# Performance work log

Measured on AMD Instinct MI355X. Metric: run time of the kernel, lower is better.

Reference implementation:

```python
import jax, jax.numpy as jnp
import numpy as np

N = 4096
D = 256
TAU = 0.8
LAM = 0.5
K0, K1 = 64, 128


def setup_inputs() -> dict:
    key = jax.random.key(0)
    ks = jax.random.split(key, 20)
    s = 1.0 / np.sqrt(D)
    pos = (jax.random.uniform(ks[3], (N, N)) < 0.01).astype(jnp.float32)
    pos = pos.at[jnp.arange(N), jnp.arange(N)].set(1.0)  # guarantee a positive per row
    return {
        'z_mp': jax.random.normal(ks[0], (N, D), jnp.float32),
        'z_sc': jax.random.normal(ks[1], (N, D), jnp.float32),
        'feat': jax.random.normal(ks[2], (N, D), jnp.float32),
        'pos': pos,
        'im2c0': jax.random.randint(ks[4], (N,), 0, K0, jnp.int32),
        'im2c1': jax.random.randint(ks[5], (N,), 0, K1, jnp.int32),
        'centroids0': jax.random.normal(ks[6], (K0, D), jnp.float32),
        'centroids1': jax.random.normal(ks[7], (K1, D), jnp.float32),
        'density0': jax.random.uniform(ks[8], (K0,), jnp.float32) + 0.5,
        'density1': jax.random.uniform(ks[9], (K1,), jnp.float32) + 0.5,
        'pW1': jax.random.normal(ks[10], (D, D), jnp.float32) * s * 1.414,
        'pb1': jnp.zeros((D,), jnp.float32),
        'pW2': jax.random.normal(ks[11], (D, D), jnp.float32) * s * 1.414,
        'pb2': jnp.zeros((D,), jnp.float32),
        'mW1': jax.random.normal(ks[12], (D, D), jnp.float32) * s,
        'mb1': jnp.zeros((D,), jnp.float32),
        'mW2': jax.random.normal(ks[13], (D, D), jnp.float32) * s,
        'mb2': jnp.zeros((D,), jnp.float32),
    }


def _mlp(x, W1, b1, W2, b2):
    # nn.Linear -> ELU -> nn.Linear (torch Linear: x @ W.T + b)
    return jax.nn.elu(x @ W1.T + b1) @ W2.T + b2


def _sim(z1, z2, tau):
    n1 = jnp.linalg.norm(z1, axis=-1, keepdims=True)
    n2 = jnp.linalg.norm(z2, axis=-1, keepdims=True)
    return jnp.exp((z1 @ z2.T) / (n1 @ n2.T) / tau)


def _nce(sim_matrix, pos):
    m = sim_matrix / (sim_matrix.sum(axis=1, keepdims=True) + 1e-8)
    return -jnp.log((m * pos).sum(axis=-1)).mean()


def _pocl(z_anchor, z, im2cs, centroids, densities):
    n = z_anchor.shape[0]
    # weight[a,b] = #levels where a,b share a cluster (original: coo @ coo.T summed)
    sames = [(c[:, None] == c[None, :]).astype(z.dtype) for c in im2cs]
    weight = sames[0] + sames[1]
    node_prototypes = jnp.zeros_like(z)
    loss = jnp.float32(0.0)
    for same, im2c, protos, dens in zip(sames, im2cs, centroids, densities):
        # original aliases weight_clus = weight, so masking accumulates in-place
        weight = weight * same
        c = (weight @ z) / weight.sum(axis=1)[:, None]
        node_prototypes = node_prototypes + 0.1 * c
        phi = dens[im2c]
        pos_p = jnp.exp((z_anchor * node_prototypes).sum(axis=1) / phi)
        neg_p = jnp.exp((z_anchor @ protos.T) / dens).mean(axis=1) * n
        loss = loss + (-jnp.log(pos_p / neg_p)).mean()
    return loss / len(im2cs)


def reference(z_mp, z_sc, feat, pos, im2c0, im2c1, centroids0, centroids1,
              density0, density1, pW1, pb1, pW2, pb2, mW1, mb1, mW2, mb2):
    z_proj_mp = _mlp(z_mp, pW1, pb1, pW2, pb2)
    z_proj_sc = _mlp(z_sc, pW1, pb1, pW2, pb2)
    m_mp2sc = _sim(z_proj_mp, z_proj_sc, TAU)
    lori_mp = _nce(m_mp2sc, pos)
    lori_sc = _nce(m_mp2sc.T, pos)
    proto_loss = _pocl(z_sc, z_mp, [im2c0, im2c1],
                       [centroids0, centroids1], [density0, density1])
    mp_intra = _mlp(z_mp, mW1, mb1, mW2, mb2)
    loss_intramp = _nce(_sim(mp_intra, mp_intra, 0.05), pos)
    proj_mp_feat = _mlp(z_mp, pW1, pb1, pW2, pb2)
    proj_feat = _mlp(feat, pW1, pb1, pW2, pb2)
    lori_mpfeat = _nce(_sim(proj_mp_feat, proj_feat, TAU), pos)
    lori_featmp = _nce(_sim(proj_feat, proj_mp_feat, TAU), pos)
    return (LAM * lori_mp + (1 - LAM) * lori_sc + 0.3 * loss_intramp
            + proto_loss + 0.01 * lori_mpfeat + 0.01 * lori_featmp)
```

## Files before the change

### kernel.cpp

```cpp
#include <hip/hip_runtime.h>
#include <math.h>


#define NROWS 4096
#define DIM   256
#define ND    ((size_t)NROWS * DIM)

typedef unsigned short u16;
typedef unsigned int   u32;
typedef unsigned long long u64;
typedef __attribute__((ext_vector_type(8))) short bf16x8;
typedef __attribute__((ext_vector_type(4))) float f32x4;

__device__ __forceinline__ u16 f2bf(float f) {
    u32 u = __float_as_uint(f);
    return (u16)((u + 0x7fffu + ((u >> 16) & 1u)) >> 16);
}
__device__ __forceinline__ float bf2f(u16 h) {
    return __uint_as_float(((u32)h) << 16);
}

__device__ __forceinline__ void gload16(const u16* g, u16* l) {
    __builtin_amdgcn_global_load_lds(
        (const __attribute__((address_space(1))) u32*)g,
        (__attribute__((address_space(3))) u32*)l, 16, 0, 0);
}

template<int ROWS>
__device__ __forceinline__ void stage_panel(const u16* P, int kk, u16* S, int tid) {
#pragma unroll
    for (int p = 0; p < ROWS / 64; ++p) {
        const int ch = p * 256 + tid, row = ch >> 2, seg = ch & 3;
        gload16(P + (size_t)row * DIM + kk + seg * 8, &S[ch * 8]);
    }
}

__device__ __forceinline__ void wait_lgkm0() {
    asm volatile("s_waitcnt lgkmcnt(0)" ::: "memory");
    __builtin_amdgcn_sched_barrier(0);
}
template<int N> __device__ __forceinline__ void wait_vm() {
    if constexpr (N == 0)      asm volatile("s_waitcnt vmcnt(0)" ::: "memory");
    else if constexpr (N == 3) asm volatile("s_waitcnt vmcnt(3)" ::: "memory");
    else if constexpr (N == 4) asm volatile("s_waitcnt vmcnt(4)" ::: "memory");
    else if constexpr (N == 6) asm volatile("s_waitcnt vmcnt(6)" ::: "memory");
}

struct Ptr3 { const float* s0; const float* s1; const float* s2; };
__global__ __launch_bounds__(256) void cvt_in(Ptr3 p, u16* __restrict__ dst)
{
    const int z = blockIdx.y;
    const float* s = z == 0 ? p.s0 : (z == 1 ? p.s1 : p.s2);
    u16* d = dst + (size_t)z * ND;
    const int i = blockIdx.x * 256 + threadIdx.x;
    const float4 v = ((const float4*)s)[i];
    ushort4 o;
    o.x = f2bf(v.x); o.y = f2bf(v.y); o.z = f2bf(v.z); o.w = f2bf(v.w);
    ((ushort4*)d)[i] = o;
}
struct Ptr4 { const float* s0; const float* s1; const float* s2; const float* s3; };
__global__ __launch_bounds__(256) void cvt_w(Ptr4 p, u16* __restrict__ dst)
{
    const int z = blockIdx.y;
    const float* s = z == 0 ? p.s0 : (z == 1 ? p.s1 : (z == 2 ? p.s2 : p.s3));
    u16* d = dst + (size_t)z * 65536;
    const int i = blockIdx.x * 256 + threadIdx.x;
    const float4 v = ((const float4*)s)[i];
    ushort4 o;
    o.x = f2bf(v.x); o.y = f2bf(v.y); o.z = f2bf(v.z); o.w = f2bf(v.w);
    ((ushort4*)d)[i] = o;
}
__global__ __launch_bounds__(256) void cvt_cent(const float* __restrict__ c0,
                                                const float* __restrict__ c1,
                                                u16* __restrict__ CB)
{
    const int i = blockIdx.x * 256 + threadIdx.x;
    const float4 v = (i < 4096) ? ((const float4*)c0)[i]
                                : ((const float4*)c1)[i - 4096];
    ushort4 o;
    o.x = f2bf(v.x); o.y = f2bf(v.y); o.z = f2bf(v.z); o.w = f2bf(v.w);
    ((ushort4*)CB)[i] = o;
}

__global__ __launch_bounds__(256) void posbits(const float* __restrict__ pos,
                                               u64* __restrict__ bits)
{
    const int i = blockIdx.x;
    const int w = threadIdx.x >> 6, l = threadIdx.x & 63;
#pragma unroll
    for (int c = 0; c < 16; ++c) {
        const int j = c * 256 + w * 64 + l;
        const float v = pos[(size_t)i * NROWS + j];
        const u64 m = __ballot(v != 0.f);
        if (l == 0) bits[(size_t)i * 64 + c * 4 + w] = m;
    }
}

template<int ACT, int REMAP>
__global__ __launch_bounds__(256, 4) void mlp_mfma(const u16* __restrict__ IN,
                                                   const u16* __restrict__ Wp,
                                                   const u16* __restrict__ Wm,
                                                   const float* __restrict__ bp,
                                                   const float* __restrict__ bm,
                                                   u16* __restrict__ OUT)
{
    __shared__ __align__(16) u16 As[3][64 * 32];
    __shared__ __align__(16) u16 Bs[3][128 * 32];
    const int tid = threadIdx.x;
    const int bx = blockIdx.x, by = blockIdx.y;
    const bool intra = by >= 192;
    const int arow = (REMAP && intra) ? (by - 192) * 64 : by * 64;
    const u16* A = IN + (size_t)arow * DIM;
    const u16* B = (intra ? Wm : Wp) + (size_t)(bx * 128) * DIM;
    const float* bias = intra ? bm : bp;
    const int l = tid & 63, w = tid >> 6, wr = w >> 1, wc = w & 1;
    const int lr = l & 15, lk = l >> 4;

    f32x4 acc[2][4] = {};
    stage_panel<64>(A, 0, As[0], tid);
    stage_panel<128>(B, 0, Bs[0], tid);
    stage_panel<64>(A, 32, As[1], tid);
    stage_panel<128>(B, 32, Bs[1], tid);
    wait_vm<3>();
    __builtin_amdgcn_s_barrier();
#pragma unroll
    for (int t = 0; t < 8; ++t) {
        bf16x8 a[2], b[4];
#pragma unroll
        for (int mi = 0; mi < 2; ++mi)
            a[mi] = *(const bf16x8*)&As[t % 3][(wr * 32 + mi * 16 + lr) * 32 + lk * 8];
#pragma unroll
        for (int ni = 0; ni < 4; ++ni)
            b[ni] = *(const bf16x8*)&Bs[t % 3][(wc * 64 + ni * 16 + lr) * 32 + lk * 8];
        if (t < 6) {
            stage_panel<64>(A, (t + 2) * 32, As[(t + 2) % 3], tid);
            stage_panel<128>(B, (t + 2) * 32, Bs[(t + 2) % 3], tid);
        }
        wait_lgkm0();
#pragma unroll
        for (int mi = 0; mi < 2; ++mi)
#pragma unroll
            for (int ni = 0; ni < 4; ++ni)
                acc[mi][ni] = __builtin_amdgcn_mfma_f32_16x16x32_bf16(a[mi], b[ni], acc[mi][ni], 0, 0, 0);
        if (t < 6)      { wait_vm<3>(); __builtin_amdgcn_s_barrier(); }
        else if (t < 7) { wait_vm<0>(); __builtin_amdgcn_s_barrier(); }
    }

    const int j0 = bx * 128;
    float bv[4];
#pragma unroll
    for (int ni = 0; ni < 4; ++ni) bv[ni] = bias[j0 + wc * 64 + ni * 16 + lr];
#pragma unroll
    for (int mi = 0; mi < 2; ++mi)
#pragma unroll
        for (int r = 0; r < 4; ++r) {
            const int row = by * 64 + wr * 32 + mi * 16 + lk * 4 + r;
#pragma unroll
            for (int ni = 0; ni < 4; ++ni) {
                float v = acc[mi][ni][r] + bv[ni];
                if (ACT) v = v > 0.f ? v : expm1f(v);
                OUT[(size_t)row * DIM + j0 + wc * 64 + ni * 16 + lr] = f2bf(v);
            }
        }
}

__global__ __launch_bounds__(256) void rownorm_bf(u16* __restrict__ X)
{
    const int w = threadIdx.x >> 6, l = threadIdx.x & 63;
    const int row = blockIdx.x * 4 + w;
    ushort4* p = (ushort4*)(X + (size_t)row * DIM) + l;
    ushort4 u = *p;
    const float a = bf2f(u.x), b = bf2f(u.y), c = bf2f(u.z), d = bf2f(u.w);
    float ss = a * a + b * b + c * c + d * d;
#pragma unroll
    for (int m = 1; m < 64; m <<= 1) ss += __shfl_xor(ss, m);
    const float inv = rsqrtf(ss);
    u.x = f2bf(a * inv); u.y = f2bf(b * inv); u.z = f2bf(c * inv); u.w = f2bf(d * inv);
    *p = u;
}

__global__ __launch_bounds__(256, 3) void simstat3c(const u16* __restrict__ PROJ,
                                                    const u64* __restrict__ bits,
                                                    float* __restrict__ ST)
{
    const int bid = blockIdx.x;
    int z, by, bx;
    if (bid < 1024) {
        z = 0;
        const int x = bid & 7, j = bid >> 3;
        by = (x >> 1) * 8 + (j >> 4);
        bx = (x & 1) * 16 + (j & 15);
    } else if (bid < 1552) {
        z = 1;
        const int u = bid - 1024;
        const int t = (u & 7) * 66 + (u >> 3);
        int r = (int)((65.0f - sqrtf(4225.0f - 8.0f * (float)t)) * 0.5f);
        int off = 32 * r - (r * (r - 1)) / 2;
        if (t < off)                   { --r; off -= 33 - r; }
        else if (t >= off + (32 - r))  { off += 32 - r; ++r; }
        by = r; bx = r + (t - off);
    } else {
        z = 2;
        const int v = bid - 1552;
        const int x = v & 7, j = v >> 3;
        by = (x >> 1) * 8 + (j >> 4);
        bx = (x & 1) * 16 + (j & 15);
    }

    __shared__ __align__(16) u16 As[3][128 * 32];
    __shared__ __align__(16) u16 Bs[3][128 * 32];
    const int tid = threadIdx.x;
    int ao, bo;
    float* rsr; float* rsc;
    switch (z) {
        case 0:  ao = 0; bo = 1; rsr = ST + 0;     rsc = ST + 8192;  break;
        case 1:  ao = 3; bo = 3; rsr = ST + 16384; rsc = ST + 16384; break;
        default: ao = 0; bo = 2; rsr = ST + 24576; rsc = ST + 32768; break;
    }
    const float invtau = (z == 1) ? 20.f : 1.25f;
    const bool docol = (z != 1) || (bx > by);
    const int i0 = by * 128, j0 = bx * 128;
    const u16* A = PROJ + (size_t)ao * ND + (size_t)i0 * DIM;
    const u16* B = PROJ + (size_t)bo * ND + (size_t)j0 * DIM;
    const int l = tid & 63, w = tid >> 6, wr = w >> 1, wc = w & 1;
    const int lr = l & 15, lk = l >> 4;

    f32x4 acc[4][4] = {};
    stage_panel<128>(A, 0, As[0], tid);
    stage_panel<128>(B, 0, Bs[0], tid);
    stage_panel<128>(A, 32, As[1], tid);
    stage_panel<128>(B, 32, Bs[1], tid);
    wait_vm<4>();
    __builtin_amdgcn_s_barrier();
#pragma unroll
    for (int t = 0; t < 8; ++t) {
        bf16x8 a[4], b[4];
#pragma unroll
        for (int mi = 0; mi < 4; ++mi)
            a[mi] = *(const bf16x8*)&As[t % 3][(wr * 64 + mi * 16 + lr) * 32 + lk * 8];
#pragma unroll
        for (int ni = 0; ni < 4; ++ni)
            b[ni] = *(const bf16x8*)&Bs[t % 3][(wc * 64 + ni * 16 + lr) * 32 + lk * 8];
        if (t < 6) {
            stage_panel<128>(A, (t + 2) * 32, As[(t + 2) % 3], tid);
            stage_panel<128>(B, (t + 2) * 32, Bs[(t + 2) % 3], tid);
        }
        wait_lgkm0();
#pragma unroll
        for (int mi = 0; mi < 4; ++mi)
#pragma unroll
            for (int ni = 0; ni < 4; ++ni)
                acc[mi][ni] = __builtin_amdgcn_mfma_f32_16x16x32_bf16(a[mi], b[ni], acc[mi][ni], 0, 0, 0);
        if (t < 6)      { wait_vm<4>(); __builtin_amdgcn_s_barrier(); }
        else if (t < 7) { wait_vm<0>(); __builtin_amdgcn_s_barrier(); }
    }

#pragma unroll
    for (int mi = 0; mi < 4; ++mi)
#pragma unroll
        for (int ni = 0; ni < 4; ++ni)
#pragma unroll
            for (int r = 0; r < 4; ++r)
                acc[mi][ni][r] = __expf(acc[mi][ni][r] * invtau);

#pragma unroll
    for (int mi = 0; mi < 4; ++mi)
#pragma unroll
        for (int r = 0; r < 4; ++r) {
            const int i = i0 + wr * 64 + mi * 16 + lk * 4 + r;
            const u64 pw = bits[(size_t)i * 64 + bx * 2 + wc];
            float rsum = 0.f, psum = 0.f;
#pragma unroll
            for (int ni = 0; ni < 4; ++ni) {
                const float ev = acc[mi][ni][r];
                rsum += ev;
                psum += ((pw >> (ni * 16 + lr)) & 1ull) ? ev : 0.f;
            }
#pragma unroll
            for (int m = 1; m < 16; m <<= 1) {
                rsum += __shfl_xor(rsum, m);
                psum += __shfl_xor(psum, m);
            }
            if (lr == 0) {
                atomicAdd(&rsr[i], rsum);
                atomicAdd(&rsr[4096 + i], psum);
            }
        }

    if (docol) {
#pragma unroll
        for (int ni = 0; ni < 4; ++ni) {
            const int j = j0 + wc * 64 + ni * 16 + lr;
            const u64 pw = bits[(size_t)j * 64 + by * 2 + wr];
            float csum = 0.f, qsum = 0.f;
#pragma unroll
            for (int mi = 0; mi < 4; ++mi)
#pragma unroll
                for (int r = 0; r < 4; ++r) {
                    const float ev = acc[mi][ni][r];
                    csum += ev;
                    qsum += ((pw >> (mi * 16 + lk * 4 + r)) & 1ull) ? ev : 0.f;
                }
            csum += __shfl_xor(csum, 16); csum += __shfl_xor(csum, 32);
            qsum += __shfl_xor(qsum, 16); qsum += __shfl_xor(qsum, 32);
            if (lk == 0) {
                atomicAdd(&rsc[j], csum);
                atomicAdd(&rsc[4096 + j], qsum);
            }
        }
    }
}

__global__ __launch_bounds__(256, 4) void gcent_mfma(const u16* __restrict__ Zb,
                                                     const u16* __restrict__ CB,
                                                     float* __restrict__ G)
{
    __shared__ __align__(16) u16 As[3][128 * 32];
    __shared__ __align__(16) u16 Bs[3][64 * 32];
    const int tid = threadIdx.x;
    const int bx = blockIdx.x, by = blockIdx.y;
    const int i0 = by * 128, j0 = bx * 64;
    const u16* A = Zb + (size_t)i0 * DIM;
    const u16* B = CB + (size_t)j0 * DIM;
    const int l = tid & 63, w = tid >> 6, wr = w >> 1, wc = w & 1;
    const int lr = l & 15, lk = l >> 4;

    f32x4 acc[4][2] = {};
    stage_panel<128>(A, 0, As[0], tid);
    stage_panel<64>(B, 0, Bs[0], tid);
    stage_panel<128>(A, 32, As[1], tid);
    stage_panel<64>(B, 32, Bs[1], tid);
    wait_vm<3>();
    __builtin_amdgcn_s_barrier();
#pragma unroll
    for (int t = 0; t < 8; ++t) {
        bf16x8 a[4], b[2];
#pragma unroll
        for (int mi = 0; mi < 4; ++mi)
            a[mi] = *(const bf16x8*)&As[t % 3][(wr * 64 + mi * 16 + lr) * 32 + lk * 8];
#pragma unroll
        for (int ni = 0; ni < 2; ++ni)
            b[ni] = *(const bf16x8*)&Bs[t % 3][(wc * 32 + ni * 16 + lr) * 32 + lk * 8];
        if (t < 6) {
            stage_panel<128>(A, (t + 2) * 32, As[(t + 2) % 3], tid);
            stage_panel<64>(B, (t + 2) * 32, Bs[(t + 2) % 3], tid);
        }
        wait_lgkm0();
#pragma unroll
        for (int mi = 0; mi < 4; ++mi)
#pragma unroll
            for (int ni = 0; ni < 2; ++ni)
                acc[mi][ni] = __builtin_amdgcn_mfma_f32_16x16x32_bf16(a[mi], b[ni], acc[mi][ni], 0, 0, 0);
        if (t < 6)      { wait_vm<3>(); __builtin_amdgcn_s_barrier(); }
        else if (t < 7) { wait_vm<0>(); __builtin_amdgcn_s_barrier(); }
    }

#pragma unroll
    for (int mi = 0; mi < 4; ++mi)
#pragma unroll
        for (int r = 0; r < 4; ++r) {
            const int row = i0 + wr * 64 + mi * 16 + lk * 4 + r;
#pragma unroll
            for (int ni = 0; ni < 2; ++ni)
                G[(size_t)row * 192 + j0 + wc * 32 + ni * 16 + lr] = acc[mi][ni][r];
        }
}

__global__ __launch_bounds__(256) void scatter_pairs(const float* __restrict__ z,
                                                     const int* __restrict__ i0a,
                                                     const int* __restrict__ i1a,
                                                     float* __restrict__ S01,
                                                     float* __restrict__ cnt01)
{
    const int b = blockIdx.x, d = threadIdx.x;
    const int p = i0a[b] * 128 + i1a[b];
    atomicAdd(&S01[(size_t)p * DIM + d], z[(size_t)b * DIM + d]);
    if (d == 0) atomicAdd(&cnt01[p], 1.f);
}

__global__ __launch_bounds__(256) void reduce_pairs(const float* __restrict__ S01,
                                                    const float* __restrict__ cnt01,
                                                    float* __restrict__ S0,
                                                    float* __restrict__ cnt0)
{
    const int k0 = blockIdx.x, d = threadIdx.x;
    float s = 0.f;
    for (int k1 = 0; k1 < 128; ++k1)
        s += S01[(size_t)(k0 * 128 + k1) * DIM + d];
    S0[(size_t)k0 * DIM + d] = s;
    __shared__ float c[128];
    if (d < 128) c[d] = cnt01[k0 * 128 + d];
    __syncthreads();
    if (d == 0) {
        float t = 0.f;
        for (int i = 0; i < 128; ++i) t += c[i];
        cnt0[k0] = t;
    }
}

__global__ __launch_bounds__(256) void pocl_row(const float* __restrict__ z_sc,
                                                const int* __restrict__ i0a,
                                                const int* __restrict__ i1a,
                                                const float* __restrict__ S0,
                                                const float* __restrict__ S01,
                                                const float* __restrict__ cnt0,
                                                const float* __restrict__ cnt01,
                                                const float* __restrict__ G,
                                                const float* __restrict__ d0,
                                                const float* __restrict__ d1,
                                                float* __restrict__ L1,
                                                float* __restrict__ L2)
{
    const int w = threadIdx.x >> 6, l = threadIdx.x & 63;
    const int a = blockIdx.x * 4 + w;
    const int k0 = i0a[a], k1 = i1a[a];
    const int p = k0 * 128 + k1;
    const float n0 = cnt0[k0], n01 = cnt01[p];
    const float inv1 = 1.f / (n0 + n01), inv2 = 1.f / n01;
    const float4 s0  = *(const float4*)&S0[(size_t)k0 * DIM + l * 4];
    const float4 s01 = *(const float4*)&S01[(size_t)p * DIM + l * 4];
    const float4 zd  = *(const float4*)&z_sc[(size_t)a * DIM + l * 4];

    float dot1 = 0.f, dot2 = 0.f;
    {
        const float c1x = (s0.x + s01.x) * inv1, c2x = s01.x * inv2;
        const float c1y = (s0.y + s01.y) * inv1, c2y = s01.y * inv2;
        const float c1z = (s0.z + s01.z) * inv1, c2z = s01.z * inv2;
        const float c1w = (s0.w + s01.w) * inv1, c2w = s01.w * inv2;
        dot1 = zd.x * c1x + zd.y * c1y + zd.z * c1z + zd.w * c1w;
        dot2 = zd.x * (c1x + c2x) + zd.y * (c1y + c2y) + zd.z * (c1z + c2z) + zd.w * (c1w + c2w);
    }
    dot1 *= 0.1f; dot2 *= 0.1f;
#pragma unroll
    for (int m = 1; m < 64; m <<= 1) {
        dot1 += __shfl_xor(dot1, m);
        dot2 += __shfl_xor(dot2, m);
    }

    const float x0 = G[(size_t)a * 192 + l] / d0[l];
    float M0 = x0;
#pragma unroll
    for (int m = 1; m < 64; m <<= 1) M0 = fmaxf(M0, __shfl_xor(M0, m));
    float e0 = __expf(x0 - M0);
#pragma unroll
    for (int m = 1; m < 64; m <<= 1) e0 += __shfl_xor(e0, m);

    const float x1a = G[(size_t)a * 192 + 64 + l] / d1[l];
    const float x1b = G[(size_t)a * 192 + 128 + l] / d1[64 + l];
    float M1 = fmaxf(x1a, x1b);
#pragma unroll
    for (int m = 1; m < 64; m <<= 1) M1 = fmaxf(M1, __shfl_xor(M1, m));
    float e1 = __expf(x1a - M1) + __expf(x1b - M1);
#pragma unroll
    for (int m = 1; m < 64; m <<= 1) e1 += __shfl_xor(e1, m);

    if (l == 0) {
        const float lneg1 = M0 + logf(e0) - logf(64.f)  + logf(4096.f);
        const float lneg2 = M1 + logf(e1) - logf(128.f) + logf(4096.f);
        L1[a] = lneg1 - dot1 / d0[k0];
        L2[a] = lneg2 - dot2 / d1[k1];
    }
}

__global__ __launch_bounds__(256) void final_reduce(const float* __restrict__ st,
                                                    const float* __restrict__ L1,
                                                    const float* __restrict__ L2,
                                                    float* __restrict__ out)
{
    const int t = threadIdx.x;
    const float* rs0 = st + 0;      const float* pr0 = st + 4096;
    const float* rs1 = st + 8192;   const float* pr1 = st + 12288;
    const float* rs2 = st + 16384;  const float* pr2 = st + 20480;
    const float* rs3 = st + 24576;  const float* pr3 = st + 28672;
    const float* rs4 = st + 32768;  const float* pr4 = st + 36864;

    float acc = 0.f;
    for (int i = t; i < NROWS; i += 256) {
        const float lmp = logf(rs0[i] + 1e-8f) - logf(pr0[i]);
        const float lsc = logf(rs1[i] + 1e-8f) - logf(pr1[i]);
        const float lin = logf(rs2[i] + 1e-8f) - logf(pr2[i]);
        const float lmf = logf(rs3[i] + 1e-8f) - logf(pr3[i]);
        const float lfm = logf(rs4[i] + 1e-8f) - logf(pr4[i]);
        acc += 0.5f * (lmp + lsc) + 0.3f * lin
             + 0.01f * (lmf + lfm) + 0.5f * (L1[i] + L2[i]);
    }
    __shared__ float red[256];
    red[t] = acc; __syncthreads();
    for (int s = 128; s > 0; s >>= 1) {
        if (t < s) red[t] += red[t + s];
        __syncthreads();
    }
    if (t == 0) out[0] = red[0] * (1.f / 4096.f);
}

extern "C" void kernel_launch(void* const* d_in, const int* in_sizes, int n_in,
                              void* d_out, int out_size, void* d_ws, size_t ws_size,
                              hipStream_t stream)
{
    const float* z_mp = (const float*)d_in[0];
    const float* z_sc = (const float*)d_in[1];
    const float* feat = (const float*)d_in[2];
    const float* pos  = (const float*)d_in[3];
    const int*   im0  = (const int*)d_in[4];
    const int*   im1  = (const int*)d_in[5];
    const float* c0   = (const float*)d_in[6];
    const float* c1   = (const float*)d_in[7];
    const float* d0   = (const float*)d_in[8];
    const float* d1   = (const float*)d_in[9];
    const float* pW1  = (const float*)d_in[10];
    const float* pb1  = (const float*)d_in[11];
    const float* pW2  = (const float*)d_in[12];
    const float* pb2  = (const float*)d_in[13];
    const float* mW1  = (const float*)d_in[14];
    const float* mb1  = (const float*)d_in[15];
    const float* mW2  = (const float*)d_in[16];
    const float* mb2  = (const float*)d_in[17];
    float* out = (float*)d_out;
    float* ws  = (float*)d_ws;
    (void)in_sizes; (void)n_in; (void)out_size; (void)ws_size;

    float* ST   = ws;
    float* S0f  = ST + 40960;
    float* CN0  = S0f + 16384;
    float* CN01 = CN0 + 64;
    float* S01f = CN01 + 8192;
    float* ZEND = S01f + (size_t)8192 * DIM;
    float* G    = ZEND;
    float* L1   = G + (size_t)NROWS * 192;
    float* L2   = L1 + NROWS;
    u64*  bits  = (u64*)(L2 + NROWS);
    u16*  INb   = (u16*)(bits + (size_t)NROWS * 64);
    u16*  Hb    = INb + 3 * ND;
    u16*  PROJ  = Hb + 4 * ND;
    u16*  Wb    = PROJ + 4 * ND;
    u16*  CB    = Wb + 4 * 65536;

    hipMemsetAsync(ws, 0, (size_t)(ZEND - ws) * sizeof(float), stream);

    const dim3 blk(256);

    Ptr3 pin{z_mp, z_sc, feat};
    cvt_in<<<dim3(1024, 3), blk, 0, stream>>>(pin, INb);
    Ptr4 pw{pW1, pW2, mW1, mW2};
    cvt_w<<<dim3(64, 4), blk, 0, stream>>>(pw, Wb);
    cvt_cent<<<48, blk, 0, stream>>>(c0, c1, CB);

    posbits<<<NROWS, blk, 0, stream>>>(pos, bits);

    mlp_mfma<1, 1><<<dim3(2, 256), blk, 0, stream>>>(INb, Wb, Wb + 2 * 65536,
                                                     pb1, mb1, Hb);
    mlp_mfma<0, 0><<<dim3(2, 256), blk, 0, stream>>>(Hb, Wb + 65536, Wb + 3 * 65536,
                                                     pb2, mb2, PROJ);
    rownorm_bf<<<4096, blk, 0, stream>>>(PROJ);

    simstat3c<<<2576, blk, 0, stream>>>(PROJ, bits, ST);

    scatter_pairs<<<NROWS, blk, 0, stream>>>(z_mp, im0, im1, S01f, CN01);
    reduce_pairs<<<64, blk, 0, stream>>>(S01f, CN01, S0f, CN0);
    gcent_mfma<<<dim3(3, 32), blk, 0, stream>>>(INb + ND, CB, G);
    pocl_row<<<1024, blk, 0, stream>>>(z_sc, im0, im1, S0f, S01f, CN0, CN01,
                                       G, d0, d1, L1, L2);

    final_reduce<<<1, blk, 0, stream>>>(ST, L1, L2, out);
}
```

Baseline: 163.9 us.

## Fuse preprocessing kernels and fold row normalization into MLP epilogue and sim kernel

Merges the input/weight/centroid conversions, pos bit-packing and pair scatter into one launch with block-range dispatch. The separate rownorm pass is removed: the second MLP epilogue accumulates squared row norms via shuffles and atomics, and simstat applies rsqrt scaling to the dot products before the exp. This saves several kernel launches and a full read-modify-write pass over PROJ. In exchange it adds atomics in the MLP epilogue, and the similarities are now computed from unnormalized bf16 values, which slightly changes rounding.

```diff
diff --git a/kernel.cpp b/kernel.cpp
--- a/kernel.cpp
+++ b/kernel.cpp
@@ -43,66 +43,73 @@
     if constexpr (N == 0)      asm volatile("s_waitcnt vmcnt(0)" ::: "memory");
     else if constexpr (N == 3) asm volatile("s_waitcnt vmcnt(3)" ::: "memory");
     else if constexpr (N == 4) asm volatile("s_waitcnt vmcnt(4)" ::: "memory");
-    else if constexpr (N == 6) asm volatile("s_waitcnt vmcnt(6)" ::: "memory");
-}
-
-struct Ptr3 { const float* s0; const float* s1; const float* s2; };
-__global__ __launch_bounds__(256) void cvt_in(Ptr3 p, u16* __restrict__ dst)
-{
-    const int z = blockIdx.y;
-    const float* s = z == 0 ? p.s0 : (z == 1 ? p.s1 : p.s2);
-    u16* d = dst + (size_t)z * ND;
-    const int i = blockIdx.x * 256 + threadIdx.x;
-    const float4 v = ((const float4*)s)[i];
-    ushort4 o;
-    o.x = f2bf(v.x); o.y = f2bf(v.y); o.z = f2bf(v.z); o.w = f2bf(v.w);
-    ((ushort4*)d)[i] = o;
-}
-struct Ptr4 { const float* s0; const float* s1; const float* s2; const float* s3; };
-__global__ __launch_bounds__(256) void cvt_w(Ptr4 p, u16* __restrict__ dst)
-{
-    const int z = blockIdx.y;
-    const float* s = z == 0 ? p.s0 : (z == 1 ? p.s1 : (z == 2 ? p.s2 : p.s3));
-    u16* d = dst + (size_t)z * 65536;
-    const int i = blockIdx.x * 256 + threadIdx.x;
-    const float4 v = ((const float4*)s)[i];
-    ushort4 o;
-    o.x = f2bf(v.x); o.y = f2bf(v.y); o.z = f2bf(v.z); o.w = f2bf(v.w);
-    ((ushort4*)d)[i] = o;
-}
-__global__ __launch_bounds__(256) void cvt_cent(const float* __restrict__ c0,
-                                                const float* __restrict__ c1,
-                                                u16* __restrict__ CB)
-{
-    const int i = blockIdx.x * 256 + threadIdx.x;
-    const float4 v = (i < 4096) ? ((const float4*)c0)[i]
-                                : ((const float4*)c1)[i - 4096];
-    ushort4 o;
-    o.x = f2bf(v.x); o.y = f2bf(v.y); o.z = f2bf(v.z); o.w = f2bf(v.w);
-    ((ushort4*)CB)[i] = o;
-}
-
-__global__ __launch_bounds__(256) void posbits(const float* __restrict__ pos,
-                                               u64* __restrict__ bits)
-{
-    const int i = blockIdx.x;
-    const int w = threadIdx.x >> 6, l = threadIdx.x & 63;
-#pragma unroll
-    for (int c = 0; c < 16; ++c) {
-        const int j = c * 256 + w * 64 + l;
-        const float v = pos[(size_t)i * NROWS + j];
-        const u64 m = __ballot(v != 0.f);
-        if (l == 0) bits[(size_t)i * 64 + c * 4 + w] = m;
-    }
-}
-
-template<int ACT, int REMAP>
+}
+
+struct PreArgs {
+    const float* in0; const float* in1; const float* in2;
+    const float* w0; const float* w1; const float* w2; const float* w3;
+    const float* c0; const float* c1;
+    const float* pos; const float* z_mp;
+    const int* im0; const int* im1;
+};
+__global__ __launch_bounds__(256) void fused_pre(PreArgs p,
+                                                 u16* __restrict__ INb,
+                                                 u16* __restrict__ Wb,
+                                                 u16* __restrict__ CB,
+                                                 u64* __restrict__ bits,
+                                                 float* __restrict__ S01,
+                                                 float* __restrict__ cnt01)
+{
+    const int b = blockIdx.x, tid = threadIdx.x;
+    if (b < 3072) {
+        const int z = b >> 10;
+        const float* s = z == 0 ? p.in0 : (z == 1 ? p.in1 : p.in2);
+        const int i = (b & 1023) * 256 + tid;
+        const float4 v = ((const float4*)s)[i];
+        ushort4 o;
+        o.x = f2bf(v.x); o.y = f2bf(v.y); o.z = f2bf(v.z); o.w = f2bf(v.w);
+        ((ushort4*)(INb + (size_t)z * ND))[i] = o;
+    } else if (b < 3328) {
+        const int q = b - 3072, wi = q >> 6;
+        const float* s = wi == 0 ? p.w0 : (wi == 1 ? p.w1 : (wi == 2 ? p.w2 : p.w3));
+        const int i = (q & 63) * 256 + tid;
+        const float4 v = ((const float4*)s)[i];
+        ushort4 o;
+        o.x = f2bf(v.x); o.y = f2bf(v.y); o.z = f2bf(v.z); o.w = f2bf(v.w);
+        ((ushort4*)(Wb + (size_t)wi * 65536))[i] = o;
+    } else if (b < 3376) {
+        const int i = (b - 3328) * 256 + tid;
+        const float4 v = (i < 4096) ? ((const float4*)p.c0)[i]
+                                    : ((const float4*)p.c1)[i - 4096];
+        ushort4 o;
+        o.x = f2bf(v.x); o.y = f2bf(v.y); o.z = f2bf(v.z); o.w = f2bf(v.w);
+        ((ushort4*)CB)[i] = o;
+    } else if (b < 7472) {
+        const int i = b - 3376;
+        const int w = tid >> 6, l = tid & 63;
+#pragma unroll
+        for (int c = 0; c < 16; ++c) {
+            const int j = c * 256 + w * 64 + l;
+            const float v = p.pos[(size_t)i * NROWS + j];
+            const u64 m = __ballot(v != 0.f);
+            if (l == 0) bits[(size_t)i * 64 + c * 4 + w] = m;
+        }
+    } else {
+        const int r = b - 7472;
+        const int pp = p.im0[r] * 128 + p.im1[r];
+        atomicAdd(&S01[(size_t)pp * DIM + tid], p.z_mp[(size_t)r * DIM + tid]);
+        if (tid == 0) atomicAdd(&cnt01[pp], 1.f);
+    }
+}
+
+template<int ACT, int REMAP, int SQ>
 __global__ __launch_bounds__(256, 4) void mlp_mfma(const u16* __restrict__ IN,
                                                    const u16* __restrict__ Wp,
                                                    const u16* __restrict__ Wm,
                                                    const float* __restrict__ bp,
                                                    const float* __restrict__ bm,
-                                                   u16* __restrict__ OUT)
+                                                   u16* __restrict__ OUT,
+                                                   float* __restrict__ SS)
 {
     __shared__ __align__(16) u16 As[3][64 * 32];
     __shared__ __align__(16) u16 Bs[3][128 * 32];
@@ -155,32 +162,28 @@
 #pragma unroll
         for (int r = 0; r < 4; ++r) {
             const int row = by * 64 + wr * 32 + mi * 16 + lk * 4 + r;
+            float v4[4], sq = 0.f;
 #pragma unroll
             for (int ni = 0; ni < 4; ++ni) {
                 float v = acc[mi][ni][r] + bv[ni];
                 if (ACT) v = v > 0.f ? v : expm1f(v);
-                OUT[(size_t)row * DIM + j0 + wc * 64 + ni * 16 + lr] = f2bf(v);
+                v4[ni] = v;
+                sq += v * v;
             }
-        }
-}
-
-__global__ __launch_bounds__(256) void rownorm_bf(u16* __restrict__ X)
-{
-    const int w = threadIdx.x >> 6, l = threadIdx.x & 63;
-    const int row = blockIdx.x * 4 + w;
-    ushort4* p = (ushort4*)(X + (size_t)row * DIM) + l;
-    ushort4 u = *p;
-    const float a = bf2f(u.x), b = bf2f(u.y), c = bf2f(u.z), d = bf2f(u.w);
-    float ss = a * a + b * b + c * c + d * d;
-#pragma unroll
-    for (int m = 1; m < 64; m <<= 1) ss += __shfl_xor(ss, m);
-    const float inv = rsqrtf(ss);
-    u.x = f2bf(a * inv); u.y = f2bf(b * inv); u.z = f2bf(c * inv); u.w = f2bf(d * inv);
-    *p = u;
+            if (SQ) {
+#pragma unroll
+                for (int m = 1; m < 16; m <<= 1) sq += __shfl_xor(sq, m);
+                if (lr == 0) atomicAdd(&SS[row], sq);
+            }
+#pragma unroll
+            for (int ni = 0; ni < 4; ++ni)
+                OUT[(size_t)row * DIM + j0 + wc * 64 + ni * 16 + lr] = f2bf(v4[ni]);
+        }
 }
 
 __global__ __launch_bounds__(256, 3) void simstat3c(const u16* __restrict__ PROJ,
                                                     const u64* __restrict__ bits,
+                                                    const float* __restrict__ SS,
                                                     float* __restrict__ ST)
 {
     const int bid = blockIdx.x;
@@ -255,13 +258,24 @@
         else if (t < 7) { wait_vm<0>(); __builtin_amdgcn_s_barrier(); }
     }
 
+    const float* ssa = SS + ao * 4096;
+    const float* ssb = SS + bo * 4096;
+    float ri[4][4], rj[4];
 #pragma unroll
     for (int mi = 0; mi < 4; ++mi)
 #pragma unroll
+        for (int r = 0; r < 4; ++r)
+            ri[mi][r] = rsqrtf(ssa[i0 + wr * 64 + mi * 16 + lk * 4 + r]) * invtau;
+#pragma unroll
+    for (int ni = 0; ni < 4; ++ni)
+        rj[ni] = rsqrtf(ssb[j0 + wc * 64 + ni * 16 + lr]);
+#pragma unroll
+    for (int mi = 0; mi < 4; ++mi)
+#pragma unroll
         for (int ni = 0; ni < 4; ++ni)
 #pragma unroll
             for (int r = 0; r < 4; ++r)
-                acc[mi][ni][r] = __expf(acc[mi][ni][r] * invtau);
+                acc[mi][ni][r] = __expf(acc[mi][ni][r] * ri[mi][r] * rj[ni]);
 
 #pragma unroll
     for (int mi = 0; mi < 4; ++mi)
@@ -364,18 +378,6 @@
             for (int ni = 0; ni < 2; ++ni)
                 G[(size_t)row * 192 + j0 + wc * 32 + ni * 16 + lr] = acc[mi][ni][r];
         }
-}
-
-__global__ __launch_bounds__(256) void scatter_pairs(const float* __restrict__ z,
-                                                     const int* __restrict__ i0a,
-                                                     const int* __restrict__ i1a,
-                                                     float* __restrict__ S01,
-                                                     float* __restrict__ cnt01)
-{
-    const int b = blockIdx.x, d = threadIdx.x;
-    const int p = i0a[b] * 128 + i1a[b];
-    atomicAdd(&S01[(size_t)p * DIM + d], z[(size_t)b * DIM + d]);
-    if (d == 0) atomicAdd(&cnt01[p], 1.f);
 }
 
 __global__ __launch_bounds__(256) void reduce_pairs(const float* __restrict__ S01,
@@ -524,7 +526,8 @@
     float* CN0  = S0f + 16384;
     float* CN01 = CN0 + 64;
     float* S01f = CN01 + 8192;
-    float* ZEND = S01f + (size_t)8192 * DIM;
+    float* SS   = S01f + (size_t)8192 * DIM;
+    float* ZEND = SS + 16384;
     float* G    = ZEND;
     float* L1   = G + (size_t)NROWS * 192;
     float* L2   = L1 + NROWS;
@@ -539,23 +542,16 @@
 
     const dim3 blk(256);
 
-    Ptr3 pin{z_mp, z_sc, feat};
-    cvt_in<<<dim3(1024, 3), blk, 0, stream>>>(pin, INb);
-    Ptr4 pw{pW1, pW2, mW1, mW2};
-    cvt_w<<<dim3(64, 4), blk, 0, stream>>>(pw, Wb);
-    cvt_cent<<<48, blk, 0, stream>>>(c0, c1, CB);
-
-    posbits<<<NROWS, blk, 0, stream>>>(pos, bits);
-
-    mlp_mfma<1, 1><<<dim3(2, 256), blk, 0, stream>>>(INb, Wb, Wb + 2 * 65536,
-                                                     pb1, mb1, Hb);
-    mlp_mfma<0, 0><<<dim3(2, 256), blk, 0, stream>>>(Hb, Wb + 65536, Wb + 3 * 65536,
-                                                     pb2, mb2, PROJ);
-    rownorm_bf<<<4096, blk, 0, stream>>>(PROJ);
-
-    simstat3c<<<2576, blk, 0, stream>>>(PROJ, bits, ST);
-
-    scatter_pairs<<<NROWS, blk, 0, stream>>>(z_mp, im0, im1, S01f, CN01);
+    PreArgs pa{z_mp, z_sc, feat, pW1, pW2, mW1, mW2, c0, c1, pos, z_mp, im0, im1};
+    fused_pre<<<11568, blk, 0, stream>>>(pa, INb, Wb, CB, bits, S01f, CN01);
+
+    mlp_mfma<1, 1, 0><<<dim3(2, 256), blk, 0, stream>>>(INb, Wb, Wb + 2 * 65536,
+                                                        pb1, mb1, Hb, nullptr);
+    mlp_mfma<0, 0, 1><<<dim3(2, 256), blk, 0, stream>>>(Hb, Wb + 65536, Wb + 3 * 65536,
+                                                        pb2, mb2, PROJ, SS);
+
+    simstat3c<<<2576, blk, 0, stream>>>(PROJ, bits, SS, ST);
+
     reduce_pairs<<<64, blk, 0, stream>>>(S01f, CN01, S0f, CN0);
     gcent_mfma<<<dim3(3, 32), blk, 0, stream>>>(INb + ND, CB, G);
     pocl_row<<<1024, blk, 0, stream>>>(z_sc, im0, im1, S0f, S01f, CN0, CN01,
```

After: 156.7 us. 4.4% less time.
